# Performance work log

Hardware: AMD Instinct MI355X
Metric: run time of the kernel (lower is better)

The kernel has to match this reference:

```python
import jax, jax.numpy as jnp
import numpy as np

D_MODEL = 1024
H = 16
DK = D_MODEL // H
S = 4096


def setup_inputs() -> dict:
    key = jax.random.key(0)
    ks = jax.random.split(key, 11)
    scale = 1.0 / np.sqrt(D_MODEL)
    return {
        "Q": jax.random.normal(ks[0], (S, D_MODEL), jnp.float32),
        "K": jax.random.normal(ks[1], (S, D_MODEL), jnp.float32),
        "V": jax.random.normal(ks[2], (S, D_MODEL), jnp.float32),
        # per-head projection weights, stacked: [h, d_model, d_k]
        "Wq": jax.random.normal(ks[3], (H, D_MODEL, DK), jnp.float32) * scale,
        "bq": jax.random.normal(ks[4], (H, DK), jnp.float32) * 0.01,
        "Wk": jax.random.normal(ks[5], (H, D_MODEL, DK), jnp.float32) * scale,
        "bk": jax.random.normal(ks[6], (H, DK), jnp.float32) * 0.01,
        "Wv": jax.random.normal(ks[7], (H, D_MODEL, DK), jnp.float32) * scale,
        "bv": jax.random.normal(ks[8], (H, DK), jnp.float32) * 0.01,
        # output projection (torch Linear convention: y = x @ Wo.T + bo)
        "Wo": jax.random.normal(ks[9], (D_MODEL, D_MODEL), jnp.float32) * scale,
        "bo": jax.random.normal(ks[10], (D_MODEL,), jnp.float32) * 0.01,
    }


def reference(Q, K, V, Wq, bq, Wk, bk, Wv, bv, Wo, bo):
    # per-head projections, vectorized over heads: [h, S, d_k]
    q = jnp.einsum("sd,hdk->hsk", Q, Wq) + bq[:, None, :]
    k = jnp.einsum("sd,hdk->hsk", K, Wk) + bk[:, None, :]
    v = jnp.einsum("sd,hdk->hsk", V, Wv) + bv[:, None, :]
    # scaled dot-product attention (full [h, S, S] scores, as in the original)
    scores = jnp.einsum("hsk,htk->hst", q, k) / jnp.sqrt(jnp.float32(DK))
    attn = jax.nn.softmax(scores, axis=-1)
    o = jnp.einsum("hst,htk->hsk", attn, v)
    # concat heads along feature dim: [S, h*d_k]
    x = jnp.transpose(o, (1, 0, 2)).reshape(S, D_MODEL)
    return x @ Wo.T + bo
```

## Files before the change

kernel.cpp:

```cpp
#include <hip/hip_runtime.h>

typedef unsigned short u16;
typedef unsigned int u32;
using f32x4 = __attribute__((ext_vector_type(4))) float;
using f32x16 = __attribute__((ext_vector_type(16))) float;
using u32x4 = __attribute__((ext_vector_type(4))) u32;
using bf16x8 = __attribute__((ext_vector_type(8))) __bf16;

#define DEV __device__ __forceinline__

DEV u16 f2bf(float f) {
  u32 x = __builtin_bit_cast(u32, f);
  return (u16)((x + 0x7fffu + ((x >> 16) & 1u)) >> 16);
}

DEV f32x4 mfma16(bf16x8 a, bf16x8 b, f32x4 c) {
  return __builtin_amdgcn_mfma_f32_16x16x32_bf16(a, b, c, 0, 0, 0);
}
DEV f32x16 mfma32(bf16x8 a, bf16x8 b, f32x16 c) {
  return __builtin_amdgcn_mfma_f32_32x32x16_bf16(a, b, c, 0, 0, 0);
}

DEV float ex2(float x) {
#if __has_builtin(__builtin_amdgcn_exp2f)
  return __builtin_amdgcn_exp2f(x);
#else
  float r;
  asm("v_exp_f32 %0, %1" : "=v"(r) : "v"(x));
  return r;
#endif
}

DEV int swz(int row, int byteInRow) {
  return row * 128 + ((((byteInRow >> 4) ^ (row & 7)) << 4) | (byteInRow & 15));
}

DEV u32 pkbf(float lo, float hi) {
  union { u32 u; __bf16 h[2]; } x;
  x.h[0] = (__bf16)lo; x.h[1] = (__bf16)hi;
  return x.u;
}

DEV void gload16(const u16* g, u16* l) {
  __builtin_amdgcn_global_load_lds((const __attribute__((address_space(1))) void*)g,
                                   (__attribute__((address_space(3))) void*)l, 16, 0, 0);
}

__global__ __launch_bounds__(256) void cvt4_kernel(const float* __restrict__ a0,
                                                   const float* __restrict__ a1,
                                                   const float* __restrict__ a2,
                                                   const float* __restrict__ a3,
                                                   u16* __restrict__ o0, u16* __restrict__ o1,
                                                   u16* __restrict__ o2, u16* __restrict__ o3) {
  int y = blockIdx.y;
  if (y == 3 && blockIdx.x >= 1024) return;
  const float* in = y == 0 ? a0 : y == 1 ? a1 : y == 2 ? a2 : a3;
  u16* out = y == 0 ? o0 : y == 1 ? o1 : y == 2 ? o2 : o3;
  int i = blockIdx.x * 256 + threadIdx.x;
  float4 v = ((const float4*)in)[i];
  ushort4 w;
  w.x = f2bf(v.x); w.y = f2bf(v.y); w.z = f2bf(v.z); w.w = f2bf(v.w);
  ((ushort4*)out)[i] = w;
}

__global__ __launch_bounds__(256) void wtrans_kernel(const float* __restrict__ Wq,
                                                     const float* __restrict__ Wk,
                                                     const float* __restrict__ Wv,
                                                     u16* __restrict__ Tq,
                                                     u16* __restrict__ Tk,
                                                     u16* __restrict__ Tv) {
  __shared__ u16 t[64][68];
  const float* W = blockIdx.z == 0 ? Wq : (blockIdx.z == 1 ? Wk : Wv);
  u16* T = blockIdx.z == 0 ? Tq : (blockIdx.z == 1 ? Tk : Tv);
  int h = blockIdx.y, d0 = blockIdx.x * 64;
  int tid = threadIdx.x;
#pragma unroll
  for (int i = 0; i < 4; ++i) {
    int c = i * 256 + tid;
    int r = c >> 4, c4 = (c & 15) * 4;
    float4 v = *(const float4*)(W + h * 65536 + (d0 + r) * 64 + c4);
    t[r][c4] = f2bf(v.x); t[r][c4 + 1] = f2bf(v.y);
    t[r][c4 + 2] = f2bf(v.z); t[r][c4 + 3] = f2bf(v.w);
  }
  __syncthreads();
#pragma unroll
  for (int i = 0; i < 4; ++i) {
    int ch = i * 256 + tid;
    int cc = ch >> 4, d4 = (ch & 15) * 4;
    ushort4 w;
    w.x = t[d4][cc]; w.y = t[d4 + 1][cc]; w.z = t[d4 + 2][cc]; w.w = t[d4 + 3][cc];
    *(ushort4*)(T + (h * 64 + cc) * 1024 + d0 + d4) = w;
  }
}

DEV void gemm128_core(const char* gA, const char* gB, u16* lA, u16* lB, f32x4 (&acc)[4][4]) {
  int tid = threadIdx.x;
  int wid = tid >> 6, lane = tid & 63, g = lane >> 4, ln = lane & 15;
  int wr = wid >> 1, wc = wid & 1;
  for (int k0 = 0; k0 < 1024; k0 += 64) {
#pragma unroll
    for (int i = 0; i < 4; ++i) {
      int c = i * 256 + tid, row = c >> 3, cc = c & 7;
      uint4 va = *(const uint4*)(gA + row * 2048 + k0 * 2 + cc * 16);
      *(uint4*)((char*)lA + swz(row, cc * 16)) = va;
      uint4 vb = *(const uint4*)(gB + row * 2048 + k0 * 2 + cc * 16);
      *(uint4*)((char*)lB + swz(row, cc * 16)) = vb;
    }
    __syncthreads();
#pragma unroll
    for (int ks = 0; ks < 2; ++ks) {
      bf16x8 af[4], bfr[4];
#pragma unroll
      for (int mt = 0; mt < 4; ++mt) {
        int row = wr * 64 + mt * 16 + ln;
        af[mt] = *(const bf16x8*)((const char*)lA + swz(row, ks * 64 + g * 16));
      }
#pragma unroll
      for (int nt = 0; nt < 4; ++nt) {
        int row = wc * 64 + nt * 16 + ln;
        bfr[nt] = *(const bf16x8*)((const char*)lB + swz(row, ks * 64 + g * 16));
      }
#pragma unroll
      for (int mt = 0; mt < 4; ++mt)
#pragma unroll
        for (int nt = 0; nt < 4; ++nt)
          acc[mt][nt] = mfma16(af[mt], bfr[nt], acc[mt][nt]);
    }
    __syncthreads();
  }
}

__global__ __launch_bounds__(256, 3) void gemm_qkv(
    const u16* __restrict__ Qb, const u16* __restrict__ Kb, const u16* __restrict__ Vb,
    const u16* __restrict__ Tq, const u16* __restrict__ Tk, const u16* __restrict__ Tv,
    const float* __restrict__ bq, const float* __restrict__ bk, const float* __restrict__ bv,
    u16* __restrict__ qh, u16* __restrict__ kh, u16* __restrict__ vTh, float sc) {
  __shared__ alignas(16) u16 lA[128 * 64];
  __shared__ alignas(16) u16 lB[128 * 64];
  int z = blockIdx.z;
  const u16* A = z == 0 ? Qb : z == 1 ? Kb : Vb;
  const u16* B = z == 0 ? Tq : z == 1 ? Tk : Tv;
  const float* bias = z == 0 ? bq : z == 1 ? bk : bv;
  int bm = blockIdx.x, bn = blockIdx.y;
  f32x4 acc[4][4] = {};
  gemm128_core((const char*)(A + bm * 131072), (const char*)(B + bn * 131072), lA, lB, acc);
  int tid = threadIdx.x;
  int wid = tid >> 6, lane = tid & 63, g = lane >> 4, ln = lane & 15;
  int wr = wid >> 1, wc = wid & 1;
  float scale = z == 0 ? sc : 1.f;
  float bv_[4];
#pragma unroll
  for (int nt = 0; nt < 4; ++nt) bv_[nt] = bias[bn * 128 + wc * 64 + nt * 16 + ln];
  if (z < 2) {
    u16* out = z == 0 ? qh : kh;
#pragma unroll
    for (int mt = 0; mt < 4; ++mt)
      for (int nt = 0; nt < 4; ++nt)
        for (int r = 0; r < 4; ++r) {
          int s = bm * 128 + wr * 64 + mt * 16 + g * 4 + r;
          int j = bn * 128 + wc * 64 + nt * 16 + ln;
          out[(j >> 6) * 262144 + s * 64 + (j & 63)] = f2bf((acc[mt][nt][r] + bv_[nt]) * scale);
        }
  } else {
#pragma unroll
    for (int mt = 0; mt < 4; ++mt)
      for (int nt = 0; nt < 4; ++nt) {
        int sb = bm * 128 + wr * 64 + mt * 16 + g * 4;
        int j = bn * 128 + wc * 64 + nt * 16 + ln;
        ushort4 w;
        w.x = f2bf(acc[mt][nt][0] + bv_[nt]);
        w.y = f2bf(acc[mt][nt][1] + bv_[nt]);
        w.z = f2bf(acc[mt][nt][2] + bv_[nt]);
        w.w = f2bf(acc[mt][nt][3] + bv_[nt]);
        *(ushort4*)(vTh + j * 4096 + sb) = w;
      }
  }
}

__global__ __launch_bounds__(256) void gemm_out(const u16* __restrict__ A,
                                                const u16* __restrict__ B,
                                                const float* __restrict__ bias,
                                                float* __restrict__ out) {
  __shared__ alignas(16) u16 lA[64 * 64];
  __shared__ alignas(16) u16 lB[128 * 64];
  int tid = threadIdx.x;
  int wid = tid >> 6, lane = tid & 63, g = lane >> 4, ln = lane & 15;
  int wr = wid >> 1, wc = wid & 1;
  int bm = blockIdx.x, bn = blockIdx.y;
  const char* gA = (const char*)(A + bm * 65536);
  const char* gB = (const char*)(B + bn * 131072);
  f32x4 acc[2][4] = {};
  for (int k0 = 0; k0 < 1024; k0 += 64) {
#pragma unroll
    for (int i = 0; i < 2; ++i) {
      int c = i * 256 + tid, row = c >> 3, cc = c & 7;
      uint4 va = *(const uint4*)(gA + row * 2048 + k0 * 2 + cc * 16);
      *(uint4*)((char*)lA + swz(row, cc * 16)) = va;
    }
#pragma unroll
    for (int i = 0; i < 4; ++i) {
      int c = i * 256 + tid, row = c >> 3, cc = c & 7;
      uint4 vb = *(const uint4*)(gB + row * 2048 + k0 * 2 + cc * 16);
      *(uint4*)((char*)lB + swz(row, cc * 16)) = vb;
    }
    __syncthreads();
#pragma unroll
    for (int ks = 0; ks < 2; ++ks) {
      bf16x8 af[2], bfr[4];
#pragma unroll
      for (int mt = 0; mt < 2; ++mt) {
        int row = wr * 32 + mt * 16 + ln;
        af[mt] = *(const bf16x8*)((const char*)lA + swz(row, ks * 64 + g * 16));
      }
#pragma unroll
      for (int nt = 0; nt < 4; ++nt) {
        int row = wc * 64 + nt * 16 + ln;
        bfr[nt] = *(const bf16x8*)((const char*)lB + swz(row, ks * 64 + g * 16));
      }
#pragma unroll
      for (int mt = 0; mt < 2; ++mt)
#pragma unroll
        for (int nt = 0; nt < 4; ++nt)
          acc[mt][nt] = mfma16(af[mt], bfr[nt], acc[mt][nt]);
    }
    __syncthreads();
  }
  float bv_[4];
#pragma unroll
  for (int nt = 0; nt < 4; ++nt) bv_[nt] = bias[bn * 128 + wc * 64 + nt * 16 + ln];
#pragma unroll
  for (int mt = 0; mt < 2; ++mt)
    for (int nt = 0; nt < 4; ++nt)
      for (int r = 0; r < 4; ++r) {
        int s = bm * 64 + wr * 32 + mt * 16 + g * 4 + r;
        int j = bn * 128 + wc * 64 + nt * 16 + ln;
        out[s * 1024 + j] = acc[mt][nt][r] + bv_[nt];
      }
}

__global__ __launch_bounds__(512, 4) void flash_attn2(const u16* __restrict__ qh,
                                                      const u16* __restrict__ kh,
                                                      const u16* __restrict__ vT,
                                                      u16* __restrict__ x) {
  __shared__ alignas(16) char smem[66048];
  u16* lK = (u16*)smem;
  u16* lV = (u16*)(smem + 32768);
  float* lbuf = (float*)(smem + 65536);
  float* mergeBuf = (float*)smem;

  int tid = threadIdx.x;
  int wid = tid >> 6, lane = tid & 63;
  int grp = wid >> 2, sw = wid & 3;
  int lq = lane & 31, hi = lane >> 5;
  int nb = (blockIdx.x & 7) * 64 + (blockIdx.x >> 3);
  int h = nb >> 5, qt = nb & 31;

  const u16* gK = kh + h * 262144 + grp * 131072;
  const u16* gV = vT + h * 262144 + grp * 2048;
  u16* lKg = lK + grp * 8192;
  u16* lVg = lV + grp * 8192;

  bf16x8 qf[4];
  {
    const u16* gQ = qh + h * 262144 + (qt * 128 + sw * 32 + lq) * 64 + hi * 8;
#pragma unroll
    for (int st = 0; st < 4; ++st) qf[st] = *(const bf16x8*)(gQ + st * 16);
  }
  f32x16 o0 = {}, o1 = {}, ol = {};
  u32x4 onesw;
  onesw[0] = onesw[1] = onesw[2] = onesw[3] = 0x3F803F80u;
  bf16x8 ones = __builtin_bit_cast(bf16x8, onesw);

  int r8 = lane >> 3, pc = lane & 7;
  int rowA = sw * 16 + r8, rowB = sw * 16 + 8 + r8;
  int sKA = rowA * 64 + ((pc ^ (rowA & 7)) << 3);
  int sKB = rowB * 64 + ((pc ^ (rowB & 7)) << 3);
  int sVA = rowA * 4096 + ((pc ^ (rowA & 7)) << 3);
  int sVB = rowB * 4096 + ((pc ^ (rowB & 7)) << 3);
  u16* dKA = lKg + (sw * 16) * 64;
  u16* dKB = lKg + (sw * 16 + 8) * 64;
  u16* dVA = lVg + (sw * 16) * 64;
  u16* dVB = lVg + (sw * 16 + 8) * 64;

  gload16(gK + sKA, dKA); gload16(gK + sKB, dKB);
  gload16(gV + sVA, dVA); gload16(gV + sVB, dVB);
  const u16 *pKA = gK + sKA + 4096, *pKB = gK + sKB + 4096;
  const u16 *pVA = gV + sVA + 64, *pVB = gV + sVB + 64;

  const int NT = 32;
  for (int t = 0; t < NT; ++t) {
    asm volatile("s_waitcnt vmcnt(0)" ::: "memory");
    __builtin_amdgcn_s_barrier();
    __builtin_amdgcn_sched_barrier(0);
    int cur = t & 1;
    if (t + 1 < NT) {
      int nxt = (cur ^ 1) * 4096;
      gload16(pKA, dKA + nxt); gload16(pKB, dKB + nxt);
      gload16(pVA, dVA + nxt); gload16(pVB, dVB + nxt);
      pKA += 4096; pKB += 4096; pVA += 64; pVB += 64;
    }
    const u16* lKc = lKg + cur * 4096;
    const u16* lVc = lVg + cur * 4096;
    f32x16 s0 = {}, s1 = {};
    __builtin_amdgcn_s_setprio(1);
#pragma unroll
    for (int st = 0; st < 4; ++st) {
      bf16x8 k0 = *(const bf16x8*)((const char*)lKc + swz(lq, st * 32 + hi * 16));
      bf16x8 k1 = *(const bf16x8*)((const char*)lKc + swz(32 + lq, st * 32 + hi * 16));
      s0 = mfma32(k0, qf[st], s0);
      s1 = mfma32(k1, qf[st], s1);
    }
    __builtin_amdgcn_s_setprio(0);
#pragma unroll
    for (int r = 0; r < 16; ++r) {
      s0[r] = ex2(s0[r]);
      s1[r] = ex2(s1[r]);
    }
    bf16x8 pa[4];
#pragma unroll
    for (int n = 0; n < 2; ++n)
#pragma unroll
      for (int b2 = 0; b2 < 2; ++b2) {
        int b = b2 * 8;
        u32x4 wv;
        if (n == 0) {
          wv[0] = pkbf(s0[b + 0], s0[b + 1]); wv[1] = pkbf(s0[b + 2], s0[b + 3]);
          wv[2] = pkbf(s0[b + 4], s0[b + 5]); wv[3] = pkbf(s0[b + 6], s0[b + 7]);
        } else {
          wv[0] = pkbf(s1[b + 0], s1[b + 1]); wv[1] = pkbf(s1[b + 2], s1[b + 3]);
          wv[2] = pkbf(s1[b + 4], s1[b + 5]); wv[3] = pkbf(s1[b + 6], s1[b + 7]);
        }
        pa[n * 2 + b2] = __builtin_bit_cast(bf16x8, wv);
      }
    __builtin_amdgcn_s_setprio(1);
#pragma unroll
    for (int st = 0; st < 4; ++st) {
      uint2 a0 = *(const uint2*)((const char*)lVc + swz(lq, st * 32 + hi * 8));
      uint2 a1 = *(const uint2*)((const char*)lVc + swz(lq, st * 32 + 16 + hi * 8));
      uint2 b0 = *(const uint2*)((const char*)lVc + swz(32 + lq, st * 32 + hi * 8));
      uint2 b1 = *(const uint2*)((const char*)lVc + swz(32 + lq, st * 32 + 16 + hi * 8));
      u32x4 w0; w0[0] = a0.x; w0[1] = a0.y; w0[2] = a1.x; w0[3] = a1.y;
      u32x4 w1; w1[0] = b0.x; w1[1] = b0.y; w1[2] = b1.x; w1[3] = b1.y;
      o0 = mfma32(pa[st], __builtin_bit_cast(bf16x8, w0), o0);
      o1 = mfma32(pa[st], __builtin_bit_cast(bf16x8, w1), o1);
      ol = mfma32(pa[st], ones, ol);
    }
    __builtin_amdgcn_s_setprio(0);
  }

  __syncthreads();
  if (grp == 1) {
#pragma unroll
    for (int r = 0; r < 16; ++r) {
      int rq = (r & 3) + 8 * (r >> 2) + 4 * hi;
      float* mb = mergeBuf + (sw * 32 + rq) * 64;
      mb[lq] = o0[r];
      mb[32 + lq] = o1[r];
      if (lq == 0) lbuf[sw * 32 + rq] = ol[r];
    }
  }
  __syncthreads();
  if (grp == 0) {
#pragma unroll
    for (int r = 0; r < 16; ++r) {
      int rq = (r & 3) + 8 * (r >> 2) + 4 * hi;
      float inv = 1.f / (ol[r] + lbuf[sw * 32 + rq]);
      const float* mb = mergeBuf + (sw * 32 + rq) * 64;
      int srow = qt * 128 + sw * 32 + rq;
      u16* xr = x + srow * 1024 + h * 64;
      xr[lq] = f2bf((o0[r] + mb[lq]) * inv);
      xr[32 + lq] = f2bf((o1[r] + mb[32 + lq]) * inv);
    }
  }
}

extern "C" void kernel_launch(void* const* d_in, const int* in_sizes, int n_in,
                              void* d_out, int out_size, void* d_ws, size_t ws_size,
                              hipStream_t stream) {
  (void)in_sizes; (void)n_in; (void)out_size; (void)ws_size;
  const float* Q  = (const float*)d_in[0];
  const float* K  = (const float*)d_in[1];
  const float* V  = (const float*)d_in[2];
  const float* Wq = (const float*)d_in[3];
  const float* bq = (const float*)d_in[4];
  const float* Wk = (const float*)d_in[5];
  const float* bk = (const float*)d_in[6];
  const float* Wv = (const float*)d_in[7];
  const float* bv = (const float*)d_in[8];
  const float* Wo = (const float*)d_in[9];
  const float* bo = (const float*)d_in[10];

  char* ws = (char*)d_ws;
  u16* Qb  = (u16*)(ws + (0ull << 20));
  u16* Kb  = (u16*)(ws + (8ull << 20));
  u16* Vb  = (u16*)(ws + (16ull << 20));
  u16* Tq  = (u16*)(ws + (24ull << 20));
  u16* Tk  = (u16*)(ws + (26ull << 20));
  u16* Tv  = (u16*)(ws + (28ull << 20));
  u16* Wob = (u16*)(ws + (30ull << 20));
  u16* qh  = (u16*)(ws + (32ull << 20));
  u16* kh  = (u16*)(ws + (40ull << 20));
  u16* vTh = (u16*)(ws + (48ull << 20));
  u16* xb  = (u16*)(ws + (56ull << 20));

  const float SC = 0.125f * 1.44269504089f;

  cvt4_kernel<<<dim3(4096, 4), 256, 0, stream>>>(Q, K, V, Wo, Qb, Kb, Vb, Wob);
  wtrans_kernel<<<dim3(16, 16, 3), 256, 0, stream>>>(Wq, Wk, Wv, Tq, Tk, Tv);

  gemm_qkv<<<dim3(32, 8, 3), 256, 0, stream>>>(Qb, Kb, Vb, Tq, Tk, Tv, bq, bk, bv,
                                               qh, kh, vTh, SC);

  flash_attn2<<<512, 512, 0, stream>>>(qh, kh, vTh, xb);

  gemm_out<<<dim3(64, 8), 256, 0, stream>>>(xb, Wob, bo, (float*)d_out);
}
```

Measured before the change: 161.9 us.

## Fuse fp32-to-bf16 conversion into QKV GEMM and stream K fragments via registers

Removes the separate conversion pass over Q, K and V: the QKV GEMM now loads fp32 activations directly and packs them to bf16 while staging into LDS, so a full write and re-read of three 16 MB inputs disappears (only Wo is still converted separately). In the attention kernel, K tiles are loaded straight from global memory into register fragments with one-tile prefetch instead of going through LDS, which halves its shared memory. The row-sum is now computed with VALU adds and a shuffle instead of an extra MFMA against a ones vector. The costs are doubled global read width inside the GEMM's load loop, more register pressure from the K prefetch, and uncoalesced-ish direct global K loads.

```diff
diff --git a/kernel.cpp b/kernel.cpp
--- a/kernel.cpp
+++ b/kernel.cpp
@@ -46,21 +46,13 @@
                                    (__attribute__((address_space(3))) void*)l, 16, 0, 0);
 }
 
-__global__ __launch_bounds__(256) void cvt4_kernel(const float* __restrict__ a0,
-                                                   const float* __restrict__ a1,
-                                                   const float* __restrict__ a2,
-                                                   const float* __restrict__ a3,
-                                                   u16* __restrict__ o0, u16* __restrict__ o1,
-                                                   u16* __restrict__ o2, u16* __restrict__ o3) {
-  int y = blockIdx.y;
-  if (y == 3 && blockIdx.x >= 1024) return;
-  const float* in = y == 0 ? a0 : y == 1 ? a1 : y == 2 ? a2 : a3;
-  u16* out = y == 0 ? o0 : y == 1 ? o1 : y == 2 ? o2 : o3;
+__global__ __launch_bounds__(256) void cvt_kernel(const float* __restrict__ in,
+                                                  u16* __restrict__ out) {
   int i = blockIdx.x * 256 + threadIdx.x;
   float4 v = ((const float4*)in)[i];
-  ushort4 w;
-  w.x = f2bf(v.x); w.y = f2bf(v.y); w.z = f2bf(v.z); w.w = f2bf(v.w);
-  ((ushort4*)out)[i] = w;
+  uint2 w;
+  w.x = pkbf(v.x, v.y); w.y = pkbf(v.z, v.w);
+  ((uint2*)out)[i] = w;
 }
 
 __global__ __launch_bounds__(256) void wtrans_kernel(const float* __restrict__ Wq,
@@ -93,60 +85,59 @@
   }
 }
 
-DEV void gemm128_core(const char* gA, const char* gB, u16* lA, u16* lB, f32x4 (&acc)[4][4]) {
-  int tid = threadIdx.x;
-  int wid = tid >> 6, lane = tid & 63, g = lane >> 4, ln = lane & 15;
-  int wr = wid >> 1, wc = wid & 1;
-  for (int k0 = 0; k0 < 1024; k0 += 64) {
-#pragma unroll
-    for (int i = 0; i < 4; ++i) {
-      int c = i * 256 + tid, row = c >> 3, cc = c & 7;
-      uint4 va = *(const uint4*)(gA + row * 2048 + k0 * 2 + cc * 16);
-      *(uint4*)((char*)lA + swz(row, cc * 16)) = va;
-      uint4 vb = *(const uint4*)(gB + row * 2048 + k0 * 2 + cc * 16);
-      *(uint4*)((char*)lB + swz(row, cc * 16)) = vb;
-    }
-    __syncthreads();
-#pragma unroll
-    for (int ks = 0; ks < 2; ++ks) {
-      bf16x8 af[4], bfr[4];
-#pragma unroll
-      for (int mt = 0; mt < 4; ++mt) {
-        int row = wr * 64 + mt * 16 + ln;
-        af[mt] = *(const bf16x8*)((const char*)lA + swz(row, ks * 64 + g * 16));
-      }
-#pragma unroll
-      for (int nt = 0; nt < 4; ++nt) {
-        int row = wc * 64 + nt * 16 + ln;
-        bfr[nt] = *(const bf16x8*)((const char*)lB + swz(row, ks * 64 + g * 16));
-      }
-#pragma unroll
-      for (int mt = 0; mt < 4; ++mt)
-#pragma unroll
-        for (int nt = 0; nt < 4; ++nt)
-          acc[mt][nt] = mfma16(af[mt], bfr[nt], acc[mt][nt]);
-    }
-    __syncthreads();
-  }
-}
-
 __global__ __launch_bounds__(256, 3) void gemm_qkv(
-    const u16* __restrict__ Qb, const u16* __restrict__ Kb, const u16* __restrict__ Vb,
+    const float* __restrict__ Qf, const float* __restrict__ Kf, const float* __restrict__ Vf,
     const u16* __restrict__ Tq, const u16* __restrict__ Tk, const u16* __restrict__ Tv,
     const float* __restrict__ bq, const float* __restrict__ bk, const float* __restrict__ bv,
     u16* __restrict__ qh, u16* __restrict__ kh, u16* __restrict__ vTh, float sc) {
   __shared__ alignas(16) u16 lA[128 * 64];
   __shared__ alignas(16) u16 lB[128 * 64];
   int z = blockIdx.z;
-  const u16* A = z == 0 ? Qb : z == 1 ? Kb : Vb;
+  const float* Af = z == 0 ? Qf : z == 1 ? Kf : Vf;
   const u16* B = z == 0 ? Tq : z == 1 ? Tk : Tv;
   const float* bias = z == 0 ? bq : z == 1 ? bk : bv;
   int bm = blockIdx.x, bn = blockIdx.y;
-  f32x4 acc[4][4] = {};
-  gemm128_core((const char*)(A + bm * 131072), (const char*)(B + bn * 131072), lA, lB, acc);
+  const float* gA = Af + bm * 131072;
+  const char* gB = (const char*)(B + bn * 131072);
   int tid = threadIdx.x;
   int wid = tid >> 6, lane = tid & 63, g = lane >> 4, ln = lane & 15;
   int wr = wid >> 1, wc = wid & 1;
+  f32x4 acc[4][4] = {};
+  for (int k0 = 0; k0 < 1024; k0 += 64) {
+#pragma unroll
+    for (int i = 0; i < 4; ++i) {
+      int c = i * 256 + tid, row = c >> 3, cc = c & 7;
+      float4 f0 = *(const float4*)(gA + row * 1024 + k0 + cc * 8);
+      float4 f1 = *(const float4*)(gA + row * 1024 + k0 + cc * 8 + 4);
+      u32x4 wv;
+      wv[0] = pkbf(f0.x, f0.y); wv[1] = pkbf(f0.z, f0.w);
+      wv[2] = pkbf(f1.x, f1.y); wv[3] = pkbf(f1.z, f1.w);
+      *(u32x4*)((char*)lA + swz(row, cc * 16)) = wv;
+      uint4 vb = *(const uint4*)(gB + row * 2048 + k0 * 2 + cc * 16);
+      *(uint4*)((char*)lB + swz(row, cc * 16)) = vb;
+    }
+    __syncthreads();
+#pragma unroll
+    for (int ks = 0; ks < 2; ++ks) {
+      bf16x8 af[4], bfr[4];
+#pragma unroll
+      for (int mt = 0; mt < 4; ++mt) {
+        int row = wr * 64 + mt * 16 + ln;
+        af[mt] = *(const bf16x8*)((const char*)lA + swz(row, ks * 64 + g * 16));
+      }
+#pragma unroll
+      for (int nt = 0; nt < 4; ++nt) {
+        int row = wc * 64 + nt * 16 + ln;
+        bfr[nt] = *(const bf16x8*)((const char*)lB + swz(row, ks * 64 + g * 16));
+      }
+#pragma unroll
+      for (int mt = 0; mt < 4; ++mt)
+#pragma unroll
+        for (int nt = 0; nt < 4; ++nt)
+          acc[mt][nt] = mfma16(af[mt], bfr[nt], acc[mt][nt]);
+    }
+    __syncthreads();
+  }
   float scale = z == 0 ? sc : 1.f;
   float bv_[4];
 #pragma unroll
@@ -238,14 +229,13 @@
       }
 }
 
-__global__ __launch_bounds__(512, 4) void flash_attn2(const u16* __restrict__ qh,
+__global__ __launch_bounds__(512, 4) void flash_attn3(const u16* __restrict__ qh,
                                                       const u16* __restrict__ kh,
                                                       const u16* __restrict__ vT,
                                                       u16* __restrict__ x) {
-  __shared__ alignas(16) char smem[66048];
-  u16* lK = (u16*)smem;
-  u16* lV = (u16*)(smem + 32768);
-  float* lbuf = (float*)(smem + 65536);
+  __shared__ alignas(16) char smem[32768 + 1024];
+  u16* lV = (u16*)smem;
+  float* lbuf = (float*)(smem + 32768);
   float* mergeBuf = (float*)smem;
 
   int tid = threadIdx.x;
@@ -257,7 +247,6 @@
 
   const u16* gK = kh + h * 262144 + grp * 131072;
   const u16* gV = vT + h * 262144 + grp * 2048;
-  u16* lKg = lK + grp * 8192;
   u16* lVg = lV + grp * 8192;
 
   bf16x8 qf[4];
@@ -266,26 +255,28 @@
 #pragma unroll
     for (int st = 0; st < 4; ++st) qf[st] = *(const bf16x8*)(gQ + st * 16);
   }
-  f32x16 o0 = {}, o1 = {}, ol = {};
-  u32x4 onesw;
-  onesw[0] = onesw[1] = onesw[2] = onesw[3] = 0x3F803F80u;
-  bf16x8 ones = __builtin_bit_cast(bf16x8, onesw);
+  f32x16 o0 = {}, o1 = {};
+  float l_run = 0.f;
 
   int r8 = lane >> 3, pc = lane & 7;
-  int rowA = sw * 16 + r8, rowB = sw * 16 + 8 + r8;
-  int sKA = rowA * 64 + ((pc ^ (rowA & 7)) << 3);
-  int sKB = rowB * 64 + ((pc ^ (rowB & 7)) << 3);
-  int sVA = rowA * 4096 + ((pc ^ (rowA & 7)) << 3);
-  int sVB = rowB * 4096 + ((pc ^ (rowB & 7)) << 3);
-  u16* dKA = lKg + (sw * 16) * 64;
-  u16* dKB = lKg + (sw * 16 + 8) * 64;
+  int rowA = sw * 16 + r8, rowB = rowA + 8;
+  const u16* pVA = gV + rowA * 4096 + ((pc ^ (rowA & 7)) << 3);
+  const u16* pVB = gV + rowB * 4096 + ((pc ^ (rowB & 7)) << 3);
   u16* dVA = lVg + (sw * 16) * 64;
-  u16* dVB = lVg + (sw * 16 + 8) * 64;
-
-  gload16(gK + sKA, dKA); gload16(gK + sKB, dKB);
-  gload16(gV + sVA, dVA); gload16(gV + sVB, dVB);
-  const u16 *pKA = gK + sKA + 4096, *pKB = gK + sKB + 4096;
-  const u16 *pVA = gV + sVA + 64, *pVB = gV + sVB + 64;
+  u16* dVB = dVA + 512;
+
+  const u16* pK = gK + lq * 64 + hi * 8;
+  bf16x8 ka[8];
+
+  gload16(pVA, dVA);
+  gload16(pVB, dVB);
+#pragma unroll
+  for (int st = 0; st < 4; ++st) {
+    ka[st * 2] = *(const bf16x8*)(pK + st * 16);
+    ka[st * 2 + 1] = *(const bf16x8*)(pK + 2048 + st * 16);
+  }
+  const u16* nK = pK + 4096;
+  pVA += 64; pVB += 64;
 
   const int NT = 32;
   for (int t = 0; t < NT; ++t) {
@@ -295,27 +286,42 @@
     int cur = t & 1;
     if (t + 1 < NT) {
       int nxt = (cur ^ 1) * 4096;
-      gload16(pKA, dKA + nxt); gload16(pKB, dKB + nxt);
-      gload16(pVA, dVA + nxt); gload16(pVB, dVB + nxt);
-      pKA += 4096; pKB += 4096; pVA += 64; pVB += 64;
-    }
-    const u16* lKc = lKg + cur * 4096;
-    const u16* lVc = lVg + cur * 4096;
+      gload16(pVA, dVA + nxt);
+      gload16(pVB, dVB + nxt);
+      pVA += 64; pVB += 64;
+    }
     f32x16 s0 = {}, s1 = {};
     __builtin_amdgcn_s_setprio(1);
 #pragma unroll
     for (int st = 0; st < 4; ++st) {
-      bf16x8 k0 = *(const bf16x8*)((const char*)lKc + swz(lq, st * 32 + hi * 16));
-      bf16x8 k1 = *(const bf16x8*)((const char*)lKc + swz(32 + lq, st * 32 + hi * 16));
-      s0 = mfma32(k0, qf[st], s0);
-      s1 = mfma32(k1, qf[st], s1);
+      s0 = mfma32(ka[st * 2], qf[st], s0);
+      s1 = mfma32(ka[st * 2 + 1], qf[st], s1);
     }
     __builtin_amdgcn_s_setprio(0);
+    if (t + 1 < NT) {
+#pragma unroll
+      for (int st = 0; st < 4; ++st) {
+        ka[st * 2] = *(const bf16x8*)(nK + st * 16);
+        ka[st * 2 + 1] = *(const bf16x8*)(nK + 2048 + st * 16);
+      }
+      nK += 4096;
+    }
 #pragma unroll
     for (int r = 0; r < 16; ++r) {
       s0[r] = ex2(s0[r]);
       s1[r] = ex2(s1[r]);
     }
+    float c0 = s0[0] + s1[0], c1 = s0[1] + s1[1];
+    float c2 = s0[2] + s1[2], c3 = s0[3] + s1[3];
+#pragma unroll
+    for (int r = 4; r < 16; r += 4) {
+      c0 += s0[r] + s1[r];
+      c1 += s0[r + 1] + s1[r + 1];
+      c2 += s0[r + 2] + s1[r + 2];
+      c3 += s0[r + 3] + s1[r + 3];
+    }
+    float sm = (c0 + c1) + (c2 + c3);
+    l_run += sm + __shfl_xor(sm, 32);
     bf16x8 pa[4];
 #pragma unroll
     for (int n = 0; n < 2; ++n)
@@ -332,6 +338,7 @@
         }
         pa[n * 2 + b2] = __builtin_bit_cast(bf16x8, wv);
       }
+    const u16* lVc = lVg + cur * 4096;
     __builtin_amdgcn_s_setprio(1);
 #pragma unroll
     for (int st = 0; st < 4; ++st) {
@@ -343,11 +350,11 @@
       u32x4 w1; w1[0] = b0.x; w1[1] = b0.y; w1[2] = b1.x; w1[3] = b1.y;
       o0 = mfma32(pa[st], __builtin_bit_cast(bf16x8, w0), o0);
       o1 = mfma32(pa[st], __builtin_bit_cast(bf16x8, w1), o1);
-      ol = mfma32(pa[st], ones, ol);
     }
     __builtin_amdgcn_s_setprio(0);
   }
 
+  if (hi == 0) lbuf[grp * 128 + sw * 32 + lq] = l_run;
   __syncthreads();
   if (grp == 1) {
 #pragma unroll
@@ -356,7 +363,6 @@
       float* mb = mergeBuf + (sw * 32 + rq) * 64;
       mb[lq] = o0[r];
       mb[32 + lq] = o1[r];
-      if (lq == 0) lbuf[sw * 32 + rq] = ol[r];
     }
   }
   __syncthreads();
@@ -364,7 +370,7 @@
 #pragma unroll
     for (int r = 0; r < 16; ++r) {
       int rq = (r & 3) + 8 * (r >> 2) + 4 * hi;
-      float inv = 1.f / (ol[r] + lbuf[sw * 32 + rq]);
+      float inv = 1.f / (lbuf[sw * 32 + rq] + lbuf[128 + sw * 32 + rq]);
       const float* mb = mergeBuf + (sw * 32 + rq) * 64;
       int srow = qt * 128 + sw * 32 + rq;
       u16* xr = x + srow * 1024 + h * 64;
@@ -391,9 +397,6 @@
   const float* bo = (const float*)d_in[10];
 
   char* ws = (char*)d_ws;
-  u16* Qb  = (u16*)(ws + (0ull << 20));
-  u16* Kb  = (u16*)(ws + (8ull << 20));
-  u16* Vb  = (u16*)(ws + (16ull << 20));
   u16* Tq  = (u16*)(ws + (24ull << 20));
   u16* Tk  = (u16*)(ws + (26ull << 20));
   u16* Tv  = (u16*)(ws + (28ull << 20));
@@ -405,13 +408,13 @@
 
   const float SC = 0.125f * 1.44269504089f;
 
-  cvt4_kernel<<<dim3(4096, 4), 256, 0, stream>>>(Q, K, V, Wo, Qb, Kb, Vb, Wob);
+  cvt_kernel<<<1024, 256, 0, stream>>>(Wo, Wob);
   wtrans_kernel<<<dim3(16, 16, 3), 256, 0, stream>>>(Wq, Wk, Wv, Tq, Tk, Tv);
 
-  gemm_qkv<<<dim3(32, 8, 3), 256, 0, stream>>>(Qb, Kb, Vb, Tq, Tk, Tv, bq, bk, bv,
+  gemm_qkv<<<dim3(32, 8, 3), 256, 0, stream>>>(Q, K, V, Tq, Tk, Tv, bq, bk, bv,
                                                qh, kh, vTh, SC);
 
-  flash_attn2<<<512, 512, 0, stream>>>(qh, kh, vTh, xb);
+  flash_attn3<<<512, 512, 0, stream>>>(qh, kh, vTh, xb);
 
   gemm_out<<<dim3(64, 8), 256, 0, stream>>>(xb, Wob, bo, (float*)d_out);
 }
```

New measurement: 294.6 us. +82.0%, slower.

## Software-pipeline flash attention so PV of previous tile overlaps QK of current

Applied to the files above, without the earlier changes.

Restructures the attention inner loop so the P·V MFMAs for tile t-1 are issued right after the QK^T MFMAs for tile t, with the exp/pack of the current scores happening afterwards and an epilogue handling the last tile. The V prefetch is split from the K prefetch and issued after a second barrier, once the previous V buffer has been consumed. The aim is to overlap the transcendental softmax work with matrix-core work and keep MFMA pipes busy. It adds an extra barrier per iteration and keeps pa live across iterations, which raises register pressure. gemm_qkv only inlines its helper, with no behaviour change.

```diff
diff --git a/kernel.cpp b/kernel.cpp
--- a/kernel.cpp
+++ b/kernel.cpp
@@ -93,43 +93,6 @@
   }
 }
 
-DEV void gemm128_core(const char* gA, const char* gB, u16* lA, u16* lB, f32x4 (&acc)[4][4]) {
-  int tid = threadIdx.x;
-  int wid = tid >> 6, lane = tid & 63, g = lane >> 4, ln = lane & 15;
-  int wr = wid >> 1, wc = wid & 1;
-  for (int k0 = 0; k0 < 1024; k0 += 64) {
-#pragma unroll
-    for (int i = 0; i < 4; ++i) {
-      int c = i * 256 + tid, row = c >> 3, cc = c & 7;
-      uint4 va = *(const uint4*)(gA + row * 2048 + k0 * 2 + cc * 16);
-      *(uint4*)((char*)lA + swz(row, cc * 16)) = va;
-      uint4 vb = *(const uint4*)(gB + row * 2048 + k0 * 2 + cc * 16);
-      *(uint4*)((char*)lB + swz(row, cc * 16)) = vb;
-    }
-    __syncthreads();
-#pragma unroll
-    for (int ks = 0; ks < 2; ++ks) {
-      bf16x8 af[4], bfr[4];
-#pragma unroll
-      for (int mt = 0; mt < 4; ++mt) {
-        int row = wr * 64 + mt * 16 + ln;
-        af[mt] = *(const bf16x8*)((const char*)lA + swz(row, ks * 64 + g * 16));
-      }
-#pragma unroll
-      for (int nt = 0; nt < 4; ++nt) {
-        int row = wc * 64 + nt * 16 + ln;
-        bfr[nt] = *(const bf16x8*)((const char*)lB + swz(row, ks * 64 + g * 16));
-      }
-#pragma unroll
-      for (int mt = 0; mt < 4; ++mt)
-#pragma unroll
-        for (int nt = 0; nt < 4; ++nt)
-          acc[mt][nt] = mfma16(af[mt], bfr[nt], acc[mt][nt]);
-    }
-    __syncthreads();
-  }
-}
-
 __global__ __launch_bounds__(256, 3) void gemm_qkv(
     const u16* __restrict__ Qb, const u16* __restrict__ Kb, const u16* __restrict__ Vb,
     const u16* __restrict__ Tq, const u16* __restrict__ Tk, const u16* __restrict__ Tv,
@@ -142,11 +105,43 @@
   const u16* B = z == 0 ? Tq : z == 1 ? Tk : Tv;
   const float* bias = z == 0 ? bq : z == 1 ? bk : bv;
   int bm = blockIdx.x, bn = blockIdx.y;
-  f32x4 acc[4][4] = {};
-  gemm128_core((const char*)(A + bm * 131072), (const char*)(B + bn * 131072), lA, lB, acc);
+  const char* gA = (const char*)(A + bm * 131072);
+  const char* gB = (const char*)(B + bn * 131072);
   int tid = threadIdx.x;
   int wid = tid >> 6, lane = tid & 63, g = lane >> 4, ln = lane & 15;
   int wr = wid >> 1, wc = wid & 1;
+  f32x4 acc[4][4] = {};
+  for (int k0 = 0; k0 < 1024; k0 += 64) {
+#pragma unroll
+    for (int i = 0; i < 4; ++i) {
+      int c = i * 256 + tid, row = c >> 3, cc = c & 7;
+      uint4 va = *(const uint4*)(gA + row * 2048 + k0 * 2 + cc * 16);
+      *(uint4*)((char*)lA + swz(row, cc * 16)) = va;
+      uint4 vb = *(const uint4*)(gB + row * 2048 + k0 * 2 + cc * 16);
+      *(uint4*)((char*)lB + swz(row, cc * 16)) = vb;
+    }
+    __syncthreads();
+#pragma unroll
+    for (int ks = 0; ks < 2; ++ks) {
+      bf16x8 af[4], bfr[4];
+#pragma unroll
+      for (int mt = 0; mt < 4; ++mt) {
+        int row = wr * 64 + mt * 16 + ln;
+        af[mt] = *(const bf16x8*)((const char*)lA + swz(row, ks * 64 + g * 16));
+      }
+#pragma unroll
+      for (int nt = 0; nt < 4; ++nt) {
+        int row = wc * 64 + nt * 16 + ln;
+        bfr[nt] = *(const bf16x8*)((const char*)lB + swz(row, ks * 64 + g * 16));
+      }
+#pragma unroll
+      for (int mt = 0; mt < 4; ++mt)
+#pragma unroll
+        for (int nt = 0; nt < 4; ++nt)
+          acc[mt][nt] = mfma16(af[mt], bfr[nt], acc[mt][nt]);
+    }
+    __syncthreads();
+  }
   float scale = z == 0 ? sc : 1.f;
   float bv_[4];
 #pragma unroll
@@ -238,7 +233,7 @@
       }
 }
 
-__global__ __launch_bounds__(512, 4) void flash_attn2(const u16* __restrict__ qh,
+__global__ __launch_bounds__(512, 4) void flash_attn4(const u16* __restrict__ qh,
                                                       const u16* __restrict__ kh,
                                                       const u16* __restrict__ vT,
                                                       u16* __restrict__ x) {
@@ -272,35 +267,35 @@
   bf16x8 ones = __builtin_bit_cast(bf16x8, onesw);
 
   int r8 = lane >> 3, pc = lane & 7;
-  int rowA = sw * 16 + r8, rowB = sw * 16 + 8 + r8;
-  int sKA = rowA * 64 + ((pc ^ (rowA & 7)) << 3);
-  int sKB = rowB * 64 + ((pc ^ (rowB & 7)) << 3);
-  int sVA = rowA * 4096 + ((pc ^ (rowA & 7)) << 3);
-  int sVB = rowB * 4096 + ((pc ^ (rowB & 7)) << 3);
+  int rowA = sw * 16 + r8, rowB = rowA + 8;
+  const u16* pKA = gK + rowA * 64 + ((pc ^ (rowA & 7)) << 3);
+  const u16* pKB = gK + rowB * 64 + ((pc ^ (rowB & 7)) << 3);
+  const u16* pVA = gV + rowA * 4096 + ((pc ^ (rowA & 7)) << 3);
+  const u16* pVB = gV + rowB * 4096 + ((pc ^ (rowB & 7)) << 3);
   u16* dKA = lKg + (sw * 16) * 64;
-  u16* dKB = lKg + (sw * 16 + 8) * 64;
+  u16* dKB = dKA + 512;
   u16* dVA = lVg + (sw * 16) * 64;
-  u16* dVB = lVg + (sw * 16 + 8) * 64;
-
-  gload16(gK + sKA, dKA); gload16(gK + sKB, dKB);
-  gload16(gV + sVA, dVA); gload16(gV + sVB, dVB);
-  const u16 *pKA = gK + sKA + 4096, *pKB = gK + sKB + 4096;
-  const u16 *pVA = gV + sVA + 64, *pVB = gV + sVB + 64;
+  u16* dVB = dVA + 512;
+
+  gload16(pKA, dKA); gload16(pKB, dKB);
+  gload16(pVA, dVA); gload16(pVB, dVB);
+  pKA += 4096; pKB += 4096;
+  pVA += 64; pVB += 64;
+
+  bf16x8 pa[4];
 
   const int NT = 32;
   for (int t = 0; t < NT; ++t) {
+    int cur = t & 1;
     asm volatile("s_waitcnt vmcnt(0)" ::: "memory");
     __builtin_amdgcn_s_barrier();
     __builtin_amdgcn_sched_barrier(0);
-    int cur = t & 1;
     if (t + 1 < NT) {
       int nxt = (cur ^ 1) * 4096;
       gload16(pKA, dKA + nxt); gload16(pKB, dKB + nxt);
-      gload16(pVA, dVA + nxt); gload16(pVB, dVB + nxt);
-      pKA += 4096; pKB += 4096; pVA += 64; pVB += 64;
+      pKA += 4096; pKB += 4096;
     }
     const u16* lKc = lKg + cur * 4096;
-    const u16* lVc = lVg + cur * 4096;
     f32x16 s0 = {}, s1 = {};
     __builtin_amdgcn_s_setprio(1);
 #pragma unroll
@@ -310,13 +305,34 @@
       s0 = mfma32(k0, qf[st], s0);
       s1 = mfma32(k1, qf[st], s1);
     }
+    if (t) {
+      const u16* lVp = lVg + (cur ^ 1) * 4096;
+#pragma unroll
+      for (int st = 0; st < 4; ++st) {
+        uint2 a0 = *(const uint2*)((const char*)lVp + swz(lq, st * 32 + hi * 8));
+        uint2 a1 = *(const uint2*)((const char*)lVp + swz(lq, st * 32 + 16 + hi * 8));
+        uint2 b0 = *(const uint2*)((const char*)lVp + swz(32 + lq, st * 32 + hi * 8));
+        uint2 b1 = *(const uint2*)((const char*)lVp + swz(32 + lq, st * 32 + 16 + hi * 8));
+        u32x4 w0; w0[0] = a0.x; w0[1] = a0.y; w0[2] = a1.x; w0[3] = a1.y;
+        u32x4 w1; w1[0] = b0.x; w1[1] = b0.y; w1[2] = b1.x; w1[3] = b1.y;
+        o0 = mfma32(pa[st], __builtin_bit_cast(bf16x8, w0), o0);
+        o1 = mfma32(pa[st], __builtin_bit_cast(bf16x8, w1), o1);
+        ol = mfma32(pa[st], ones, ol);
+      }
+    }
     __builtin_amdgcn_s_setprio(0);
+    __builtin_amdgcn_s_barrier();
+    __builtin_amdgcn_sched_barrier(0);
+    if (t + 1 < NT) {
+      int nxt = (cur ^ 1) * 4096;
+      gload16(pVA, dVA + nxt); gload16(pVB, dVB + nxt);
+      pVA += 64; pVB += 64;
+    }
 #pragma unroll
     for (int r = 0; r < 16; ++r) {
       s0[r] = ex2(s0[r]);
       s1[r] = ex2(s1[r]);
     }
-    bf16x8 pa[4];
 #pragma unroll
     for (int n = 0; n < 2; ++n)
 #pragma unroll
@@ -332,13 +348,16 @@
         }
         pa[n * 2 + b2] = __builtin_bit_cast(bf16x8, wv);
       }
+  }
+  {
+    const u16* lVp = lVg + ((NT - 1) & 1) * 4096;
     __builtin_amdgcn_s_setprio(1);
 #pragma unroll
     for (int st = 0; st < 4; ++st) {
-      uint2 a0 = *(const uint2*)((const char*)lVc + swz(lq, st * 32 + hi * 8));
-      uint2 a1 = *(const uint2*)((const char*)lVc + swz(lq, st * 32 + 16 + hi * 8));
-      uint2 b0 = *(const uint2*)((const char*)lVc + swz(32 + lq, st * 32 + hi * 8));
-      uint2 b1 = *(const uint2*)((const char*)lVc + swz(32 + lq, st * 32 + 16 + hi * 8));
+      uint2 a0 = *(const uint2*)((const char*)lVp + swz(lq, st * 32 + hi * 8));
+      uint2 a1 = *(const uint2*)((const char*)lVp + swz(lq, st * 32 + 16 + hi * 8));
+      uint2 b0 = *(const uint2*)((const char*)lVp + swz(32 + lq, st * 32 + hi * 8));
+      uint2 b1 = *(const uint2*)((const char*)lVp + swz(32 + lq, st * 32 + 16 + hi * 8));
       u32x4 w0; w0[0] = a0.x; w0[1] = a0.y; w0[2] = a1.x; w0[3] = a1.y;
       u32x4 w1; w1[0] = b0.x; w1[1] = b0.y; w1[2] = b1.x; w1[3] = b1.y;
       o0 = mfma32(pa[st], __builtin_bit_cast(bf16x8, w0), o0);
@@ -411,7 +430,7 @@
   gemm_qkv<<<dim3(32, 8, 3), 256, 0, stream>>>(Qb, Kb, Vb, Tq, Tk, Tv, bq, bk, bv,
                                                qh, kh, vTh, SC);
 
-  flash_attn2<<<512, 512, 0, stream>>>(qh, kh, vTh, xb);
+  flash_attn4<<<512, 512, 0, stream>>>(qh, kh, vTh, xb);
 
   gemm_out<<<dim3(64, 8), 256, 0, stream>>>(xb, Wob, bo, (float*)d_out);
 }
```

Result: slower. 177.7 us (+9.8%).
